# Kernel optimization log

Hardware: AMD Instinct MI355X
Metric: run time of the kernel (lower is better)

## Reference

```python
import jax, jax.numpy as jnp
import numpy as np

EMB = 1024
HEADS = 16
HEAD_DIM = EMB // HEADS


def setup_inputs() -> dict:
    key = jax.random.key(0)
    ks = jax.random.split(key, 11)
    B, S = 4, 2048
    scale = 1.0 / np.sqrt(EMB)
    inp = {
        "query": jax.random.normal(ks[0], (B, S, EMB), jnp.float32),
        "key": jax.random.normal(ks[1], (B, S, EMB), jnp.float32),
        "value": jax.random.normal(ks[2], (B, S, EMB), jnp.float32),
        "Wq": jax.random.normal(ks[3], (EMB, EMB), jnp.float32) * scale,
        "bq": jnp.zeros((EMB,), jnp.float32),
        "Wk": jax.random.normal(ks[4], (EMB, EMB), jnp.float32) * scale,
        "bk": jnp.zeros((EMB,), jnp.float32),
        "Wv": jax.random.normal(ks[5], (EMB, EMB), jnp.float32) * scale,
        "bv": jnp.zeros((EMB,), jnp.float32),
        "Wo": jax.random.normal(ks[6], (EMB, EMB), jnp.float32) * scale,
        "bo": jnp.zeros((EMB,), jnp.float32),
    }
    return inp


def reference(query, key, value, Wq, bq, Wk, bk, Wv, bv, Wo, bo):
    B, S, E = query.shape
    H, D = HEADS, HEAD_DIM

    def split_heads(x):  # [B,S,E] -> [B,H,S,D]
        return x.reshape(B, -1, H, D).transpose(0, 2, 1, 3)

    Q = split_heads(query @ Wq + bq)
    K = split_heads(key @ Wk + bk)
    V = split_heads(value @ Wv + bv)

    scores = jnp.einsum("bhqd,bhkd->bhqk", Q, K) / jnp.sqrt(jnp.float32(D))
    attn = jax.nn.softmax(scores, axis=-1)
    out = jnp.einsum("bhqk,bhkd->bhqd", attn, V)
    out = out.transpose(0, 2, 1, 3).reshape(B, S, E)
    return out @ Wo + bo
```

## Files before the change

kernel.cpp:

```cpp
#include <hip/hip_runtime.h>

typedef unsigned short ushort_t;
typedef __attribute__((ext_vector_type(8))) short bf16x8;
typedef __attribute__((ext_vector_type(4))) float f32x4;
typedef __attribute__((ext_vector_type(16))) float f32x16;
typedef __attribute__((ext_vector_type(4))) int i32x4;
typedef __attribute__((ext_vector_type(2))) unsigned int u32x2;

#define QSCALE 0.1803368801111204f

__device__ inline ushort_t f2bf(float f) {
    unsigned int u = __float_as_uint(f);
    unsigned int r = (u + 0x7FFFu + ((u >> 16) & 1u)) >> 16;
    return (ushort_t)r;
}
__device__ inline unsigned pkbf(float x, float y) {
    unsigned d;
    asm("v_cvt_pk_bf16_f32 %0, %1, %2" : "=v"(d) : "v"(x), "v"(y));
    return d;
}
__device__ inline bf16x8 frag_from(unsigned a, unsigned b, unsigned c, unsigned d) {
    union { i32x4 i; bf16x8 v; } u;
    u.i[0] = (int)a; u.i[1] = (int)b; u.i[2] = (int)c; u.i[3] = (int)d;
    return u.v;
}

__device__ inline bf16x8 mkfrag(float x0, float x1, float x2, float x3,
                                float x4, float x5, float x6, float x7, int hi) {
    unsigned A_ = pkbf(x0, x1), B_ = pkbf(x2, x3), C_ = pkbf(x4, x5), D_ = pkbf(x6, x7);
    unsigned Ax = (unsigned)__shfl_xor((int)A_, 32);
    unsigned Bx = (unsigned)__shfl_xor((int)B_, 32);
    unsigned Cx = (unsigned)__shfl_xor((int)C_, 32);
    unsigned Dx = (unsigned)__shfl_xor((int)D_, 32);
    return frag_from(hi ? Cx : A_, hi ? Dx : B_, hi ? C_ : Ax, hi ? D_ : Bx);
}

__global__ __launch_bounds__(256) void transpose_cast4(
    const float* __restrict__ W0, const float* __restrict__ W1,
    const float* __restrict__ W2, const float* __restrict__ W3,
    ushort_t* __restrict__ T0, ushort_t* __restrict__ T1,
    ushort_t* __restrict__ T2, ushort_t* __restrict__ T3) {
    __shared__ float tile[32][33];
    const int which = blockIdx.x >> 10;
    const float* W = which == 0 ? W0 : which == 1 ? W1 : which == 2 ? W2 : W3;
    ushort_t* Wt = which == 0 ? T0 : which == 1 ? T1 : which == 2 ? T2 : T3;
    const int bidx = blockIdx.x & 1023;
    const int bx = bidx & 31, by = bidx >> 5;
    const int n0 = bx * 32, k0 = by * 32;
    const int tx = threadIdx.x & 31, ty = threadIdx.x >> 5;
#pragma unroll
    for (int i = 0; i < 4; ++i) {
        int r = ty + i * 8;
        tile[r][tx] = W[(k0 + r) * 1024 + n0 + tx];
    }
    __syncthreads();
#pragma unroll
    for (int i = 0; i < 4; ++i) {
        int r = ty + i * 8;
        Wt[(n0 + r) * 1024 + k0 + tx] = f2bf(tile[tx][r]);
    }
}

__global__ __launch_bounds__(256) void v_transpose(const ushort_t* __restrict__ Vp,
                                                   ushort_t* __restrict__ Vt) {
    __shared__ alignas(16) ushort_t tile[64][72];
    const int bid = blockIdx.x;
    const int pair = bid >> 5, st0 = (bid & 31) * 64;
    const ushort_t* src = Vp + (size_t)pair * 2048 * 64;
    ushort_t* dst = Vt + (size_t)pair * 64 * 2048;
    const int t = threadIdx.x;
    const int sl = t >> 2, d0 = (t & 3) * 16;
    *(bf16x8*)&tile[sl][d0] = *(const bf16x8*)&src[(size_t)(st0 + sl) * 64 + d0];
    *(bf16x8*)&tile[sl][d0 + 8] = *(const bf16x8*)&src[(size_t)(st0 + sl) * 64 + d0 + 8];
    __syncthreads();
    const int dl = t >> 2, s0 = (t & 3) * 16;
    bf16x8 a, b;
#pragma unroll
    for (int j = 0; j < 8; ++j) {
        a[j] = (short)tile[s0 + j][dl];
        b[j] = (short)tile[s0 + 8 + j][dl];
    }
    *(bf16x8*)&dst[(size_t)dl * 2048 + st0 + s0] = a;
    *(bf16x8*)&dst[(size_t)dl * 2048 + st0 + s0 + 8] = b;
}

template <int AF32, int OMODE>
__global__ __launch_bounds__(256) void gemm_bt(const void* __restrict__ Ap,
                                               const ushort_t* __restrict__ Bt,
                                               const float* __restrict__ bias,
                                               void* __restrict__ out, float scale) {
    __shared__ alignas(16) ushort_t As[128 * 72];
    __shared__ alignas(16) ushort_t Bs[128 * 72];
    const int t = threadIdx.x;
    const int lane = t & 63, w = t >> 6;
    const int q = lane & 15, g = lane >> 4;
    const int wr = w >> 1, wc = w & 1;
    const int bm = blockIdx.x & 63, bn = blockIdx.x >> 6;
    const int m0 = bm * 128, n0 = bn * 128;

    f32x4 acc[4][4];
#pragma unroll
    for (int i = 0; i < 4; ++i)
#pragma unroll
        for (int j = 0; j < 4; ++j) acc[i][j] = (f32x4){0.f, 0.f, 0.f, 0.f};

    for (int k0 = 0; k0 < 1024; k0 += 64) {
        __syncthreads();
#pragma unroll
        for (int it = 0; it < 4; ++it) {
            int tt = t + it * 256;
            int row = tt >> 3;
            int col = (tt & 7) * 8;
            if (AF32) {
                const float* A = (const float*)Ap;
                float4 v0 = *(const float4*)&A[(size_t)(m0 + row) * 1024 + k0 + col];
                float4 v1 = *(const float4*)&A[(size_t)(m0 + row) * 1024 + k0 + col + 4];
                *(bf16x8*)&As[row * 72 + col] =
                    frag_from(pkbf(v0.x, v0.y), pkbf(v0.z, v0.w),
                              pkbf(v1.x, v1.y), pkbf(v1.z, v1.w));
            } else {
                const ushort_t* A = (const ushort_t*)Ap;
                *(bf16x8*)&As[row * 72 + col] =
                    *(const bf16x8*)&A[(size_t)(m0 + row) * 1024 + k0 + col];
            }
            *(bf16x8*)&Bs[row * 72 + col] =
                *(const bf16x8*)&Bt[(size_t)(n0 + row) * 1024 + k0 + col];
        }
        __syncthreads();
#pragma unroll
        for (int kt = 0; kt < 2; ++kt) {
            bf16x8 af[4], bfr[4];
#pragma unroll
            for (int mt = 0; mt < 4; ++mt)
                af[mt] = *(const bf16x8*)&As[(wr * 64 + mt * 16 + q) * 72 + kt * 32 + g * 8];
#pragma unroll
            for (int nt = 0; nt < 4; ++nt)
                bfr[nt] = *(const bf16x8*)&Bs[(wc * 64 + nt * 16 + q) * 72 + kt * 32 + g * 8];
#pragma unroll
            for (int mt = 0; mt < 4; ++mt)
#pragma unroll
                for (int nt = 0; nt < 4; ++nt)
                    acc[mt][nt] = __builtin_amdgcn_mfma_f32_16x16x32_bf16(
                        af[mt], bfr[nt], acc[mt][nt], 0, 0, 0);
        }
    }

#pragma unroll
    for (int mt = 0; mt < 4; ++mt) {
#pragma unroll
        for (int nt = 0; nt < 4; ++nt) {
#pragma unroll
            for (int r = 0; r < 4; ++r) {
                int grow = m0 + wr * 64 + mt * 16 + g * 4 + r;
                int col = n0 + wc * 64 + nt * 16 + q;
                float v = acc[mt][nt][r] + bias[col];
                if (OMODE == 0) {
                    int b = grow >> 11, s = grow & 2047;
                    int h = col >> 6, d = col & 63;
                    ((ushort_t*)out)[(((size_t)(b * 16 + h) * 2048 + s) * 64) + d] =
                        f2bf(v * scale);
                } else {
                    ((float*)out)[(size_t)grow * 1024 + col] = v;
                }
            }
        }
    }
}

__global__ __launch_bounds__(512, 4) void attn_kernel(const ushort_t* __restrict__ Qp,
                                                      const ushort_t* __restrict__ Kp,
                                                      const ushort_t* __restrict__ Vtp,
                                                      ushort_t* __restrict__ Oa) {
    __shared__ alignas(16) ushort_t Ks[2][4096];
    __shared__ alignas(16) ushort_t Vs[2][4096];

    const int t = threadIdx.x, lane = t & 63, w = t >> 6;
    const int li = lane & 31, hi = lane >> 5;
    const int bid = (blockIdx.x & 7) * 64 + (blockIdx.x >> 3);
    const int pair = bid >> 3;
    const int qbase = (bid & 7) * 256 + w * 32;

    const ushort_t* Qh = Qp + (size_t)pair * 2048 * 64;
    const ushort_t* Kh = Kp + (size_t)pair * 2048 * 64;
    const ushort_t* Vh = Vtp + (size_t)pair * 64 * 2048;

    bf16x8 qf[4];
#pragma unroll
    for (int ks = 0; ks < 4; ++ks)
        qf[ks] = *(const bf16x8*)&Qh[(size_t)(qbase + li) * 64 + ks * 16 + hi * 8];

    const short one_bf = (short)0x3F80;
    const bf16x8 onesf = {one_bf, one_bf, one_bf, one_bf, one_bf, one_bf, one_bf, one_bf};

    f32x16 o0 = {0.f,0.f,0.f,0.f,0.f,0.f,0.f,0.f,0.f,0.f,0.f,0.f,0.f,0.f,0.f,0.f};
    f32x16 o1 = {0.f,0.f,0.f,0.f,0.f,0.f,0.f,0.f,0.f,0.f,0.f,0.f,0.f,0.f,0.f,0.f};
    f32x16 osum = {0.f,0.f,0.f,0.f,0.f,0.f,0.f,0.f,0.f,0.f,0.f,0.f,0.f,0.f,0.f,0.f};
    float m_ = -1e30f;

    const int r8 = t >> 3;
    const int lcol = (t & 7) * 16;
    const int swoff = (r8 * 128) + (lcol ^ ((r8 & 7) << 4));
    const char* kp0 = (const char*)Kh + (size_t)r8 * 128 + lcol;
    const char* vp0 = (const char*)Vh + (size_t)r8 * 4096 + lcol;
    char* KsB = (char*)Ks;
    char* VsB = (char*)Vs;
    const int sw = (li & 7) << 4;

    i32x4 gk0 = *(const i32x4*)(kp0);
    i32x4 gv0 = *(const i32x4*)(vp0);
    *(i32x4*)(KsB + swoff) = gk0;
    *(i32x4*)(VsB + swoff) = gv0;
    gk0 = *(const i32x4*)(kp0 + 8192);
    gv0 = *(const i32x4*)(vp0 + 128);
    __syncthreads();

    for (int it = 0; it < 32; ++it) {
        const int cur = it & 1;
        if (it < 31) {
            const int nb = (cur ^ 1) * 8192;
            *(i32x4*)(KsB + nb + swoff) = gk0;
            *(i32x4*)(VsB + nb + swoff) = gv0;
        }
        if (it < 30) {
            gk0 = *(const i32x4*)(kp0 + (size_t)(it + 2) * 8192);
            gv0 = *(const i32x4*)(vp0 + (size_t)(it + 2) * 128);
        }

        const char* kb = KsB + cur * 8192;
        const char* vb = VsB + cur * 8192;

        f32x16 s0 = {0.f,0.f,0.f,0.f,0.f,0.f,0.f,0.f,0.f,0.f,0.f,0.f,0.f,0.f,0.f,0.f};
        f32x16 s1 = {0.f,0.f,0.f,0.f,0.f,0.f,0.f,0.f,0.f,0.f,0.f,0.f,0.f,0.f,0.f,0.f};
        __builtin_amdgcn_s_setprio(1);
#pragma unroll
        for (int ks = 0; ks < 4; ++ks) {
            const int b = ks * 32 + hi * 16;
            bf16x8 k0 = *(const bf16x8*)(kb + li * 128 + (b ^ sw));
            bf16x8 k1 = *(const bf16x8*)(kb + (32 + li) * 128 + (b ^ sw));
            s0 = __builtin_amdgcn_mfma_f32_32x32x16_bf16(k0, qf[ks], s0, 0, 0, 0);
            s1 = __builtin_amdgcn_mfma_f32_32x32x16_bf16(k1, qf[ks], s1, 0, 0, 0);
        }
        __builtin_amdgcn_s_setprio(0);

        float mx[8];
#pragma unroll
        for (int j = 0; j < 8; ++j)
            mx[j] = fmaxf(fmaxf(s0[j], s0[j + 8]), fmaxf(s1[j], s1[j + 8]));
        float m01 = fmaxf(mx[0], mx[1]), m23 = fmaxf(mx[2], mx[3]);
        float m45 = fmaxf(mx[4], mx[5]), m67 = fmaxf(mx[6], mx[7]);
        float tm = fmaxf(fmaxf(m01, m23), fmaxf(m45, m67));
        tm = fmaxf(tm, __shfl_xor(tm, 32));
        if (__any(tm > m_ + 8.f)) {
            float mn = fmaxf(m_, tm);
            float corr = exp2f(m_ - mn);
#pragma unroll
            for (int r = 0; r < 16; ++r) { o0[r] *= corr; o1[r] *= corr; }
            osum[0] *= corr;
            m_ = mn;
        }
#pragma unroll
        for (int r = 0; r < 16; ++r) s0[r] = exp2f(s0[r] - m_);
#pragma unroll
        for (int r = 0; r < 16; ++r) s1[r] = exp2f(s1[r] - m_);

        bf16x8 pf[4];
        pf[0] = mkfrag(s0[0], s0[1], s0[2], s0[3], s0[4], s0[5], s0[6], s0[7], hi);
        pf[1] = mkfrag(s0[8], s0[9], s0[10], s0[11], s0[12], s0[13], s0[14], s0[15], hi);
        pf[2] = mkfrag(s1[0], s1[1], s1[2], s1[3], s1[4], s1[5], s1[6], s1[7], hi);
        pf[3] = mkfrag(s1[8], s1[9], s1[10], s1[11], s1[12], s1[13], s1[14], s1[15], hi);

        __builtin_amdgcn_s_setprio(1);
#pragma unroll
        for (int ks = 0; ks < 4; ++ks) {
            const int b = ks * 32 + hi * 16;
            bf16x8 v0 = *(const bf16x8*)(vb + li * 128 + (b ^ sw));
            bf16x8 v1 = *(const bf16x8*)(vb + (32 + li) * 128 + (b ^ sw));
            o0 = __builtin_amdgcn_mfma_f32_32x32x16_bf16(v0, pf[ks], o0, 0, 0, 0);
            o1 = __builtin_amdgcn_mfma_f32_32x32x16_bf16(v1, pf[ks], o1, 0, 0, 0);
            osum = __builtin_amdgcn_mfma_f32_32x32x16_bf16(onesf, pf[ks], osum, 0, 0, 0);
        }
        __builtin_amdgcn_s_setprio(0);

        __syncthreads();
    }

    const float rl = 1.0f / osum[0];
    const int b = pair >> 4, hh = pair & 15;
    const int s = qbase + li;
    const size_t rowbase = ((size_t)(b * 2048 + s)) * 1024 + hh * 64;
#pragma unroll
    for (int dt = 0; dt < 2; ++dt) {
#pragma unroll
        for (int rq = 0; rq < 4; ++rq) {
            float v0 = (dt ? o1[rq * 4 + 0] : o0[rq * 4 + 0]) * rl;
            float v1 = (dt ? o1[rq * 4 + 1] : o0[rq * 4 + 1]) * rl;
            float v2 = (dt ? o1[rq * 4 + 2] : o0[rq * 4 + 2]) * rl;
            float v3 = (dt ? o1[rq * 4 + 3] : o0[rq * 4 + 3]) * rl;
            u32x2 uv;
            uv[0] = pkbf(v0, v1);
            uv[1] = pkbf(v2, v3);
            *(u32x2*)&Oa[rowbase + dt * 32 + rq * 8 + hi * 4] = uv;
        }
    }
}

extern "C" void kernel_launch(void* const* d_in, const int* in_sizes, int n_in,
                              void* d_out, int out_size, void* d_ws, size_t ws_size,
                              hipStream_t stream) {
    const float* query = (const float*)d_in[0];
    const float* key_ = (const float*)d_in[1];
    const float* value = (const float*)d_in[2];
    const float* Wq = (const float*)d_in[3];
    const float* bq = (const float*)d_in[4];
    const float* Wk = (const float*)d_in[5];
    const float* bk = (const float*)d_in[6];
    const float* Wv = (const float*)d_in[7];
    const float* bv = (const float*)d_in[8];
    const float* Wo = (const float*)d_in[9];
    const float* bo = (const float*)d_in[10];
    float* out = (float*)d_out;

    char* ws = (char*)d_ws;
    ushort_t* Wqt = (ushort_t*)(ws + 0);
    ushort_t* Wkt = (ushort_t*)(ws + 2097152);
    ushort_t* Wvt = (ushort_t*)(ws + 4194304);
    ushort_t* Wot = (ushort_t*)(ws + 6291456);
    ushort_t* Qp = (ushort_t*)(ws + 8388608);
    ushort_t* Kp = (ushort_t*)(ws + 25165824);
    ushort_t* Vp = (ushort_t*)(ws + 41943040);
    ushort_t* Vt = (ushort_t*)(ws + 58720256);
    ushort_t* Oa = (ushort_t*)(ws + 41943040);

    transpose_cast4<<<4096, 256, 0, stream>>>(Wq, Wk, Wv, Wo, Wqt, Wkt, Wvt, Wot);

    gemm_bt<1, 0><<<512, 256, 0, stream>>>((const void*)query, Wqt, bq, (void*)Qp, QSCALE);
    gemm_bt<1, 0><<<512, 256, 0, stream>>>((const void*)key_, Wkt, bk, (void*)Kp, 1.0f);
    gemm_bt<1, 0><<<512, 256, 0, stream>>>((const void*)value, Wvt, bv, (void*)Vp, 1.0f);

    v_transpose<<<2048, 256, 0, stream>>>(Vp, Vt);

    attn_kernel<<<512, 512, 0, stream>>>(Qp, Kp, Vt, Oa);

    gemm_bt<0, 1><<<512, 256, 0, stream>>>((const void*)Oa, Wot, bo, (void*)out, 1.0f);
}
```

Before: 250.9 us.

## Stream K/V tiles via direct global-to-LDS loads and compute row sums on VALU

```diff
diff --git a/kernel.cpp b/kernel.cpp
--- a/kernel.cpp
+++ b/kernel.cpp
@@ -18,6 +18,11 @@
     unsigned d;
     asm("v_cvt_pk_bf16_f32 %0, %1, %2" : "=v"(d) : "v"(x), "v"(y));
     return d;
+}
+__device__ inline float vexp2(float x) {
+    float r;
+    asm("v_exp_f32 %0, %1" : "=v"(r) : "v"(x));
+    return r;
 }
 __device__ inline bf16x8 frag_from(unsigned a, unsigned b, unsigned c, unsigned d) {
     union { i32x4 i; bf16x8 v; } u;
@@ -189,51 +194,51 @@
     for (int ks = 0; ks < 4; ++ks)
         qf[ks] = *(const bf16x8*)&Qh[(size_t)(qbase + li) * 64 + ks * 16 + hi * 8];
 
-    const short one_bf = (short)0x3F80;
-    const bf16x8 onesf = {one_bf, one_bf, one_bf, one_bf, one_bf, one_bf, one_bf, one_bf};
-
-    f32x16 o0 = {0.f,0.f,0.f,0.f,0.f,0.f,0.f,0.f,0.f,0.f,0.f,0.f,0.f,0.f,0.f,0.f};
-    f32x16 o1 = {0.f,0.f,0.f,0.f,0.f,0.f,0.f,0.f,0.f,0.f,0.f,0.f,0.f,0.f,0.f,0.f};
-    f32x16 osum = {0.f,0.f,0.f,0.f,0.f,0.f,0.f,0.f,0.f,0.f,0.f,0.f,0.f,0.f,0.f,0.f};
-    float m_ = -1e30f;
-
-    const int r8 = t >> 3;
-    const int lcol = (t & 7) * 16;
-    const int swoff = (r8 * 128) + (lcol ^ ((r8 & 7) << 4));
-    const char* kp0 = (const char*)Kh + (size_t)r8 * 128 + lcol;
-    const char* vp0 = (const char*)Vh + (size_t)r8 * 4096 + lcol;
+    const f32x16 z16 = {0.f,0.f,0.f,0.f,0.f,0.f,0.f,0.f,0.f,0.f,0.f,0.f,0.f,0.f,0.f,0.f};
+    f32x16 o0 = z16, o1 = z16;
+    float m_ = -1e30f, l_ = 0.f;
+
+    const int srow = w * 8 + (lane >> 3);
+    const int scol = ((lane & 7) ^ (srow & 7)) << 4;
+    const char* kgp = (const char*)Kh + (size_t)srow * 128 + scol;
+    const char* vgp = (const char*)Vh + (size_t)srow * 4096 + scol;
     char* KsB = (char*)Ks;
     char* VsB = (char*)Vs;
     const int sw = (li & 7) << 4;
 
-    i32x4 gk0 = *(const i32x4*)(kp0);
-    i32x4 gv0 = *(const i32x4*)(vp0);
-    *(i32x4*)(KsB + swoff) = gk0;
-    *(i32x4*)(VsB + swoff) = gv0;
-    gk0 = *(const i32x4*)(kp0 + 8192);
-    gv0 = *(const i32x4*)(vp0 + 128);
+#define STAGE(buf, tile)                                                          \
+    do {                                                                          \
+        __builtin_amdgcn_global_load_lds(                                         \
+            (const __attribute__((address_space(1))) void*)(kgp + (size_t)(tile) * 8192), \
+            (__attribute__((address_space(3))) void*)(KsB + (buf) * 8192 + w * 1024),     \
+            16, 0, 0);                                                            \
+        __builtin_amdgcn_global_load_lds(                                         \
+            (const __attribute__((address_space(1))) void*)(vgp + (size_t)(tile) * 128),  \
+            (__attribute__((address_space(3))) void*)(VsB + (buf) * 8192 + w * 1024),     \
+            16, 0, 0);                                                            \
+    } while (0)
+
+    STAGE(0, 0);
     __syncthreads();
 
     for (int it = 0; it < 32; ++it) {
         const int cur = it & 1;
-        if (it < 31) {
-            const int nb = (cur ^ 1) * 8192;
-            *(i32x4*)(KsB + nb + swoff) = gk0;
-            *(i32x4*)(VsB + nb + swoff) = gv0;
-        }
-        if (it < 30) {
-            gk0 = *(const i32x4*)(kp0 + (size_t)(it + 2) * 8192);
-            gv0 = *(const i32x4*)(vp0 + (size_t)(it + 2) * 128);
-        }
+        if (it < 31) STAGE(cur ^ 1, it + 1);
 
         const char* kb = KsB + cur * 8192;
         const char* vb = VsB + cur * 8192;
 
-        f32x16 s0 = {0.f,0.f,0.f,0.f,0.f,0.f,0.f,0.f,0.f,0.f,0.f,0.f,0.f,0.f,0.f,0.f};
-        f32x16 s1 = {0.f,0.f,0.f,0.f,0.f,0.f,0.f,0.f,0.f,0.f,0.f,0.f,0.f,0.f,0.f,0.f};
+        f32x16 s0, s1;
         __builtin_amdgcn_s_setprio(1);
-#pragma unroll
-        for (int ks = 0; ks < 4; ++ks) {
+        {
+            const int b = hi * 16;
+            bf16x8 k0 = *(const bf16x8*)(kb + li * 128 + (b ^ sw));
+            bf16x8 k1 = *(const bf16x8*)(kb + (32 + li) * 128 + (b ^ sw));
+            s0 = __builtin_amdgcn_mfma_f32_32x32x16_bf16(k0, qf[0], z16, 0, 0, 0);
+            s1 = __builtin_amdgcn_mfma_f32_32x32x16_bf16(k1, qf[0], z16, 0, 0, 0);
+        }
+#pragma unroll
+        for (int ks = 1; ks < 4; ++ks) {
             const int b = ks * 32 + hi * 16;
             bf16x8 k0 = *(const bf16x8*)(kb + li * 128 + (b ^ sw));
             bf16x8 k1 = *(const bf16x8*)(kb + (32 + li) * 128 + (b ^ sw));
@@ -252,16 +257,25 @@
         tm = fmaxf(tm, __shfl_xor(tm, 32));
         if (__any(tm > m_ + 8.f)) {
             float mn = fmaxf(m_, tm);
-            float corr = exp2f(m_ - mn);
+            float corr = vexp2(m_ - mn);
 #pragma unroll
             for (int r = 0; r < 16; ++r) { o0[r] *= corr; o1[r] *= corr; }
-            osum[0] *= corr;
+            l_ *= corr;
             m_ = mn;
         }
 #pragma unroll
-        for (int r = 0; r < 16; ++r) s0[r] = exp2f(s0[r] - m_);
-#pragma unroll
-        for (int r = 0; r < 16; ++r) s1[r] = exp2f(s1[r] - m_);
+        for (int r = 0; r < 16; ++r) s0[r] = vexp2(s0[r] - m_);
+#pragma unroll
+        for (int r = 0; r < 16; ++r) s1[r] = vexp2(s1[r] - m_);
+        float su[8];
+#pragma unroll
+        for (int j = 0; j < 8; ++j)
+            su[j] = (s0[j] + s0[j + 8]) + (s1[j] + s1[j + 8]);
+        float s01 = su[0] + su[1], s23 = su[2] + su[3];
+        float s45 = su[4] + su[5], s67 = su[6] + su[7];
+        float sum = (s01 + s23) + (s45 + s67);
+        sum += __shfl_xor(sum, 32);
+        l_ += sum;
 
         bf16x8 pf[4];
         pf[0] = mkfrag(s0[0], s0[1], s0[2], s0[3], s0[4], s0[5], s0[6], s0[7], hi);
@@ -277,14 +291,14 @@
             bf16x8 v1 = *(const bf16x8*)(vb + (32 + li) * 128 + (b ^ sw));
             o0 = __builtin_amdgcn_mfma_f32_32x32x16_bf16(v0, pf[ks], o0, 0, 0, 0);
             o1 = __builtin_amdgcn_mfma_f32_32x32x16_bf16(v1, pf[ks], o1, 0, 0, 0);
-            osum = __builtin_amdgcn_mfma_f32_32x32x16_bf16(onesf, pf[ks], osum, 0, 0, 0);
         }
         __builtin_amdgcn_s_setprio(0);
 
         __syncthreads();
     }
-
-    const float rl = 1.0f / osum[0];
+#undef STAGE
+
+    const float rl = 1.0f / l_;
     const int b = pair >> 4, hh = pair & 15;
     const int s = qbase + li;
     const size_t rowbase = ((size_t)(b * 2048 + s)) * 1024 + hh * 64;
```

Result: faster. 227.6 us (-9.3%).

## Write V transposed from projection GEMM, compute softmax row sum in registers

Applied to the files above, without the earlier changes.

```diff
diff --git a/kernel.cpp b/kernel.cpp
--- a/kernel.cpp
+++ b/kernel.cpp
@@ -18,6 +18,11 @@
     unsigned d;
     asm("v_cvt_pk_bf16_f32 %0, %1, %2" : "=v"(d) : "v"(x), "v"(y));
     return d;
+}
+__device__ inline float vexp2(float x) {
+    float r;
+    asm("v_exp_f32 %0, %1" : "=v"(r) : "v"(x));
+    return r;
 }
 __device__ inline bf16x8 frag_from(unsigned a, unsigned b, unsigned c, unsigned d) {
     union { i32x4 i; bf16x8 v; } u;
@@ -59,29 +64,6 @@
         int r = ty + i * 8;
         Wt[(n0 + r) * 1024 + k0 + tx] = f2bf(tile[tx][r]);
     }
-}
-
-__global__ __launch_bounds__(256) void v_transpose(const ushort_t* __restrict__ Vp,
-                                                   ushort_t* __restrict__ Vt) {
-    __shared__ alignas(16) ushort_t tile[64][72];
-    const int bid = blockIdx.x;
-    const int pair = bid >> 5, st0 = (bid & 31) * 64;
-    const ushort_t* src = Vp + (size_t)pair * 2048 * 64;
-    ushort_t* dst = Vt + (size_t)pair * 64 * 2048;
-    const int t = threadIdx.x;
-    const int sl = t >> 2, d0 = (t & 3) * 16;
-    *(bf16x8*)&tile[sl][d0] = *(const bf16x8*)&src[(size_t)(st0 + sl) * 64 + d0];
-    *(bf16x8*)&tile[sl][d0 + 8] = *(const bf16x8*)&src[(size_t)(st0 + sl) * 64 + d0 + 8];
-    __syncthreads();
-    const int dl = t >> 2, s0 = (t & 3) * 16;
-    bf16x8 a, b;
-#pragma unroll
-    for (int j = 0; j < 8; ++j) {
-        a[j] = (short)tile[s0 + j][dl];
-        b[j] = (short)tile[s0 + 8 + j][dl];
-    }
-    *(bf16x8*)&dst[(size_t)dl * 2048 + st0 + s0] = a;
-    *(bf16x8*)&dst[(size_t)dl * 2048 + st0 + s0 + 8] = b;
 }
 
 template <int AF32, int OMODE>
@@ -149,18 +131,32 @@
     for (int mt = 0; mt < 4; ++mt) {
 #pragma unroll
         for (int nt = 0; nt < 4; ++nt) {
-#pragma unroll
-            for (int r = 0; r < 4; ++r) {
-                int grow = m0 + wr * 64 + mt * 16 + g * 4 + r;
-                int col = n0 + wc * 64 + nt * 16 + q;
-                float v = acc[mt][nt][r] + bias[col];
-                if (OMODE == 0) {
-                    int b = grow >> 11, s = grow & 2047;
-                    int h = col >> 6, d = col & 63;
-                    ((ushort_t*)out)[(((size_t)(b * 16 + h) * 2048 + s) * 64) + d] =
-                        f2bf(v * scale);
-                } else {
-                    ((float*)out)[(size_t)grow * 1024 + col] = v;
+            const int col = n0 + wc * 64 + nt * 16 + q;
+            if (OMODE == 2) {
+                const int grow0 = m0 + wr * 64 + mt * 16 + g * 4;
+                const int b = grow0 >> 11, si = grow0 & 2047;
+                const int h = col >> 6, d = col & 63;
+                float v0 = (acc[mt][nt][0] + bias[col]) * scale;
+                float v1 = (acc[mt][nt][1] + bias[col]) * scale;
+                float v2 = (acc[mt][nt][2] + bias[col]) * scale;
+                float v3 = (acc[mt][nt][3] + bias[col]) * scale;
+                u32x2 uv;
+                uv[0] = pkbf(v0, v1);
+                uv[1] = pkbf(v2, v3);
+                *(u32x2*)&((ushort_t*)out)[((size_t)((b * 16 + h) * 64 + d)) * 2048 + si] = uv;
+            } else {
+#pragma unroll
+                for (int r = 0; r < 4; ++r) {
+                    int grow = m0 + wr * 64 + mt * 16 + g * 4 + r;
+                    float v = acc[mt][nt][r] + bias[col];
+                    if (OMODE == 0) {
+                        int b = grow >> 11, s = grow & 2047;
+                        int h = col >> 6, d = col & 63;
+                        ((ushort_t*)out)[(((size_t)(b * 16 + h) * 2048 + s) * 64) + d] =
+                            f2bf(v * scale);
+                    } else {
+                        ((float*)out)[(size_t)grow * 1024 + col] = v;
+                    }
                 }
             }
         }
@@ -189,13 +185,9 @@
     for (int ks = 0; ks < 4; ++ks)
         qf[ks] = *(const bf16x8*)&Qh[(size_t)(qbase + li) * 64 + ks * 16 + hi * 8];
 
-    const short one_bf = (short)0x3F80;
-    const bf16x8 onesf = {one_bf, one_bf, one_bf, one_bf, one_bf, one_bf, one_bf, one_bf};
-
-    f32x16 o0 = {0.f,0.f,0.f,0.f,0.f,0.f,0.f,0.f,0.f,0.f,0.f,0.f,0.f,0.f,0.f,0.f};
-    f32x16 o1 = {0.f,0.f,0.f,0.f,0.f,0.f,0.f,0.f,0.f,0.f,0.f,0.f,0.f,0.f,0.f,0.f};
-    f32x16 osum = {0.f,0.f,0.f,0.f,0.f,0.f,0.f,0.f,0.f,0.f,0.f,0.f,0.f,0.f,0.f,0.f};
-    float m_ = -1e30f;
+    const f32x16 z16 = {0.f,0.f,0.f,0.f,0.f,0.f,0.f,0.f,0.f,0.f,0.f,0.f,0.f,0.f,0.f,0.f};
+    f32x16 o0 = z16, o1 = z16;
+    float m_ = -1e30f, l_ = 0.f;
 
     const int r8 = t >> 3;
     const int lcol = (t & 7) * 16;
@@ -229,8 +221,7 @@
         const char* kb = KsB + cur * 8192;
         const char* vb = VsB + cur * 8192;
 
-        f32x16 s0 = {0.f,0.f,0.f,0.f,0.f,0.f,0.f,0.f,0.f,0.f,0.f,0.f,0.f,0.f,0.f,0.f};
-        f32x16 s1 = {0.f,0.f,0.f,0.f,0.f,0.f,0.f,0.f,0.f,0.f,0.f,0.f,0.f,0.f,0.f,0.f};
+        f32x16 s0 = z16, s1 = z16;
         __builtin_amdgcn_s_setprio(1);
 #pragma unroll
         for (int ks = 0; ks < 4; ++ks) {
@@ -252,16 +243,25 @@
         tm = fmaxf(tm, __shfl_xor(tm, 32));
         if (__any(tm > m_ + 8.f)) {
             float mn = fmaxf(m_, tm);
-            float corr = exp2f(m_ - mn);
+            float corr = vexp2(m_ - mn);
 #pragma unroll
             for (int r = 0; r < 16; ++r) { o0[r] *= corr; o1[r] *= corr; }
-            osum[0] *= corr;
+            l_ *= corr;
             m_ = mn;
         }
 #pragma unroll
-        for (int r = 0; r < 16; ++r) s0[r] = exp2f(s0[r] - m_);
-#pragma unroll
-        for (int r = 0; r < 16; ++r) s1[r] = exp2f(s1[r] - m_);
+        for (int r = 0; r < 16; ++r) s0[r] = vexp2(s0[r] - m_);
+#pragma unroll
+        for (int r = 0; r < 16; ++r) s1[r] = vexp2(s1[r] - m_);
+        float su[8];
+#pragma unroll
+        for (int j = 0; j < 8; ++j)
+            su[j] = (s0[j] + s0[j + 8]) + (s1[j] + s1[j + 8]);
+        float s01 = su[0] + su[1], s23 = su[2] + su[3];
+        float s45 = su[4] + su[5], s67 = su[6] + su[7];
+        float sum = (s01 + s23) + (s45 + s67);
+        sum += __shfl_xor(sum, 32);
+        l_ += sum;
 
         bf16x8 pf[4];
         pf[0] = mkfrag(s0[0], s0[1], s0[2], s0[3], s0[4], s0[5], s0[6], s0[7], hi);
@@ -277,14 +277,13 @@
             bf16x8 v1 = *(const bf16x8*)(vb + (32 + li) * 128 + (b ^ sw));
             o0 = __builtin_amdgcn_mfma_f32_32x32x16_bf16(v0, pf[ks], o0, 0, 0, 0);
             o1 = __builtin_amdgcn_mfma_f32_32x32x16_bf16(v1, pf[ks], o1, 0, 0, 0);
-            osum = __builtin_amdgcn_mfma_f32_32x32x16_bf16(onesf, pf[ks], osum, 0, 0, 0);
         }
         __builtin_amdgcn_s_setprio(0);
 
         __syncthreads();
     }
 
-    const float rl = 1.0f / osum[0];
+    const float rl = 1.0f / l_;
     const int b = pair >> 4, hh = pair & 15;
     const int s = qbase + li;
     const size_t rowbase = ((size_t)(b * 2048 + s)) * 1024 + hh * 64;
@@ -327,7 +326,6 @@
     ushort_t* Wot = (ushort_t*)(ws + 6291456);
     ushort_t* Qp = (ushort_t*)(ws + 8388608);
     ushort_t* Kp = (ushort_t*)(ws + 25165824);
-    ushort_t* Vp = (ushort_t*)(ws + 41943040);
     ushort_t* Vt = (ushort_t*)(ws + 58720256);
     ushort_t* Oa = (ushort_t*)(ws + 41943040);
 
@@ -335,9 +333,7 @@
 
     gemm_bt<1, 0><<<512, 256, 0, stream>>>((const void*)query, Wqt, bq, (void*)Qp, QSCALE);
     gemm_bt<1, 0><<<512, 256, 0, stream>>>((const void*)key_, Wkt, bk, (void*)Kp, 1.0f);
-    gemm_bt<1, 0><<<512, 256, 0, stream>>>((const void*)value, Wvt, bv, (void*)Vp, 1.0f);
-
-    v_transpose<<<2048, 256, 0, stream>>>(Vp, Vt);
+    gemm_bt<1, 2><<<512, 256, 0, stream>>>((const void*)value, Wvt, bv, (void*)Vt, 1.0f);
 
     attn_kernel<<<512, 512, 0, stream>>>(Qp, Kp, Vt, Oa);
 
```

After: 225.2 us. -10.3%, faster.
